# Kernel tuning notes

Hardware: AMD Instinct MI355X
Metric: run time of the kernel (lower is better)

Reference implementation:

```python
import jax, jax.numpy as jnp
import numpy as np

N_EMB = 1024
N_HEADS = 16
HS = N_EMB // N_HEADS  # 64
BASE = 10000.0


def _rope_cache(T):
    # theta uses dim = n_emb (as in the source), sliced to hs//2 frequencies
    i = jnp.arange(HS // 2, dtype=jnp.float32)
    theta = BASE ** (-2.0 * i / N_EMB)            # [hs/2]
    pos = jnp.arange(T, dtype=jnp.float32)        # [T]
    ang = pos[:, None] * theta[None, :]           # [T, hs/2]
    return jnp.cos(ang), jnp.sin(ang)


def _apply_rope(x, cos, sin):
    # x: [B, T, nh, hs]; rotate consecutive pairs along hs
    b, t, nh, hs = x.shape
    xr = x.reshape(b, t, nh, hs // 2, 2)
    c = cos[None, :, None, :]
    s = sin[None, :, None, :]
    r0 = xr[..., 0] * c - xr[..., 1] * s
    r1 = xr[..., 1] * c + xr[..., 0] * s
    return jnp.stack([r0, r1], axis=-1).reshape(b, t, nh, hs)


def setup_inputs() -> dict:
    key = jax.random.key(0)
    k1, k2, k3, k4 = jax.random.split(key, 4)
    B, T = 2, 2048
    w_std = 0.02
    x = jax.random.normal(k1, (B, T, N_EMB), jnp.float32)
    Wq = jax.random.normal(k2, (N_EMB, N_EMB), jnp.float32) * w_std
    Wk = jax.random.normal(k3, (N_EMB, N_EMB), jnp.float32) * w_std
    Wv = jax.random.normal(k4, (N_EMB, N_EMB), jnp.float32) * w_std
    return {"x": x, "Wq": Wq, "Wk": Wk, "Wv": Wv}


def reference(x, Wq, Wk, Wv):
    B, T, C = x.shape
    # nn.Linear(bias=False): y = x @ W.T
    q = (x @ Wq.T).reshape(B, T, N_HEADS, HS)
    k = (x @ Wk.T).reshape(B, T, N_HEADS, HS)
    v = (x @ Wv.T).reshape(B, T, N_HEADS, HS)
    cos, sin = _rope_cache(T)
    q = _apply_rope(q, cos, sin)
    k = _apply_rope(k, cos, sin)
    # scale uses C (n_emb), as in the source (not head_size)
    wei = jnp.einsum('bqhd,bkhd->bhqk', q, k) * (C ** -0.5)  # [B, nh, T, T]
    mask = jnp.tril(jnp.ones((T, T), dtype=bool))
    wei = jnp.where(mask[None, None], wei, -jnp.inf)
    wei = jax.nn.softmax(wei, axis=-1)
    # dropout is identity in eval mode
    out = jnp.einsum('bhqk,bkhd->bqhd', wei, v).reshape(B, T, C)
    return out
```

## Files before the change

kernel.cpp:

```cpp
#include <hip/hip_runtime.h>
#include <stdint.h>

typedef unsigned short u16;
typedef __bf16 bf16x8 __attribute__((ext_vector_type(8)));
typedef unsigned short u16x8 __attribute__((ext_vector_type(8)));
typedef unsigned short u16x4 __attribute__((ext_vector_type(4)));
typedef float f32x4 __attribute__((ext_vector_type(4)));
typedef uint32_t u32v4 __attribute__((ext_vector_type(4)));

#define LOG2E 1.4426950408889634f

typedef const __attribute__((address_space(1))) uint32_t as1_u32;
typedef __attribute__((address_space(3))) uint32_t as3_u32;

__device__ __forceinline__ u16 f2bf(float f) {
  union { float f; uint32_t i; } v; v.f = f;
  uint32_t r = (v.i + 0x7fffu + ((v.i >> 16) & 1u)) >> 16;
  return (u16)r;
}
__device__ __forceinline__ float bf2f(u16 u) {
  union { uint32_t i; float f; } v; v.i = ((uint32_t)u) << 16; return v.f;
}

__device__ __forceinline__ void gld_lds16(const void* g, void* l) {
  as1_u32* gp = (as1_u32*)((uintptr_t)g);
  as3_u32* lp = (as3_u32*)(uint32_t)(uintptr_t)(l);
  __builtin_amdgcn_global_load_lds(gp, lp, 16, 0, 0);
}

__global__ __launch_bounds__(256) void f32_to_bf16(
    const float* __restrict__ x, const float* __restrict__ wq,
    const float* __restrict__ wk, const float* __restrict__ wv,
    u16* __restrict__ xc, u16* __restrict__ wqc,
    u16* __restrict__ wkc, u16* __restrict__ wvc) {
  const int z = blockIdx.y;
  const float* src = z == 0 ? x : (z == 1 ? wq : (z == 2 ? wk : wv));
  u16* dst = z == 0 ? xc : (z == 1 ? wqc : (z == 2 ? wkc : wvc));
  const int n = z == 0 ? (1 << 22) : (1 << 20);

  const int idx = (blockIdx.x * 256 + (int)threadIdx.x) * 8;
  if (idx >= n) return;
  const f32x4 a = *(const f32x4*)&src[idx];
  const f32x4 b = *(const f32x4*)&src[idx + 4];
  u16x8 o;
#pragma unroll
  for (int j = 0; j < 4; j++) { o[j] = f2bf(a[j]); o[j + 4] = f2bf(b[j]); }
  *(u16x8*)&dst[idx] = o;
}

__global__ __launch_bounds__(256) void qkv_gemm(
    const u16* __restrict__ xc, const u16* __restrict__ wqc,
    const u16* __restrict__ wkc, const u16* __restrict__ wvc,
    u16* __restrict__ qo, u16* __restrict__ ko, u16* __restrict__ vt) {
  __shared__ __align__(16) u16 As[128 * 32];
  __shared__ __align__(16) u16 Bs[128 * 32];

  const int tid = threadIdx.x;
  const int lane = tid & 63;
  const int w = tid >> 6;
  const int wm = w >> 1, wn = w & 1;
  const int quad = lane >> 4, m16 = lane & 15;
  const int which = blockIdx.z;

  const u16* __restrict__ Ap;
  const u16* __restrict__ Bp;
  int m0, n0;
  if (which == 2) {
    Ap = wvc; Bp = xc;
    m0 = blockIdx.x * 128;
    n0 = blockIdx.y * 128;
  } else {
    Ap = xc; Bp = which == 0 ? wqc : wkc;
    m0 = blockIdx.y * 128;
    n0 = blockIdx.x * 128;
  }

  const f32x4 z4 = {0.f, 0.f, 0.f, 0.f};
  f32x4 acc[4][4];
#pragma unroll
  for (int i = 0; i < 4; i++)
#pragma unroll
    for (int j = 0; j < 4; j++) acc[i][j] = z4;

  const int rowA = m0 + w * 32 + (lane >> 2);
  const int rowB = n0 + w * 32 + (lane >> 2);
  const int cch = (lane & 3) * 8;

  for (int k0 = 0; k0 < 1024; k0 += 32) {
    __syncthreads();
#pragma unroll
    for (int i = 0; i < 2; i++) {
      gld_lds16(&Ap[(size_t)(rowA + i * 16) * 1024 + k0 + cch],
                &As[(w * 32 + i * 16) * 32]);
      gld_lds16(&Bp[(size_t)(rowB + i * 16) * 1024 + k0 + cch],
                &Bs[(w * 32 + i * 16) * 32]);
    }
    __syncthreads();

    bf16x8 af[4], bfr[4];
#pragma unroll
    for (int t = 0; t < 4; t++) {
      af[t]  = *(const bf16x8*)&As[(wm * 64 + t * 16 + m16) * 32 + quad * 8];
      bfr[t] = *(const bf16x8*)&Bs[(wn * 64 + t * 16 + m16) * 32 + quad * 8];
    }
#pragma unroll
    for (int mt = 0; mt < 4; mt++)
#pragma unroll
      for (int nt = 0; nt < 4; nt++)
        acc[mt][nt] = __builtin_amdgcn_mfma_f32_16x16x32_bf16(
            af[mt], bfr[nt], acc[mt][nt], 0, 0, 0);
  }

  if (which < 2) {
    u16* __restrict__ out = which == 0 ? qo : ko;
#pragma unroll
    for (int mt = 0; mt < 4; mt++) {
      const int row = m0 + wm * 64 + mt * 16 + quad * 4;
#pragma unroll
      for (int nt = 0; nt < 4; nt++) {
        const int n = n0 + wn * 64 + nt * 16 + m16;
        f32x4 a = acc[mt][nt];
#pragma unroll
        for (int r = 0; r < 4; r++)
          out[(size_t)(row + r) * 1024 + n] = f2bf(a[r]);
      }
    }
  } else {
#pragma unroll
    for (int mt = 0; mt < 4; mt++) {
      const int row = m0 + wm * 64 + mt * 16 + quad * 4;
#pragma unroll
      for (int nt = 0; nt < 4; nt++) {
        const int n = n0 + wn * 64 + nt * 16 + m16;
        f32x4 a = acc[mt][nt];
#pragma unroll
        for (int r = 0; r < 4; r++)
          vt[(size_t)(row + r) * 4096 + n] = f2bf(a[r]);
      }
    }
  }
}

__global__ __launch_bounds__(256) void rope_inplace(u16* __restrict__ qb,
                                                    u16* __restrict__ kb) {
  u16* buf = blockIdx.y == 0 ? qb : kb;
  const int p = blockIdx.x * 256 + (int)threadIdx.x;
  const int nidx = p * 2;
  const int row = nidx >> 10;
  const int col = nidx & 1023;
  const int i = (col & 63) >> 1;
  const int t = row & 2047;
  const float theta = exp2f(-(float)i * 0.02595256324130752f);
  const float ang = (float)t * theta;
  float s, c;
  sincosf(ang, &s, &c);
  const float a0 = bf2f(buf[(size_t)row * 1024 + col]);
  const float a1 = bf2f(buf[(size_t)row * 1024 + col + 1]);
  buf[(size_t)row * 1024 + col]     = f2bf(a0 * c - a1 * s);
  buf[(size_t)row * 1024 + col + 1] = f2bf(a1 * c + a0 * s);
}

__global__ __launch_bounds__(256, 4) void flash_attn(
    const u16* __restrict__ qg, const u16* __restrict__ kg,
    const u16* __restrict__ vt, float* __restrict__ out) {
  __shared__ __align__(16) u16 Ks[128 * 72];
  __shared__ __align__(16) u16 Vs[64 * 136];

  const int tid = threadIdx.x, lane = tid & 63, w = tid >> 6;
  const int quad = lane >> 4, m16 = lane & 15;

  const int id  = (int)blockIdx.x;
  const int wid = (id & 7) * 128 + (id >> 3);
  const int uu  = wid & 31;
  const int v   = wid >> 5;
  const int qt  = (v & 1) ? (31 - uu) : uu;
  const int h   = v & 15;
  const int b   = v >> 4;

  const size_t base = (size_t)b * 2048 * 1024 + (size_t)h * 64;
  const size_t vbase = (size_t)(h * 64) * 4096 + (size_t)b * 2048;
  const float SC = 0.03125f * LOG2E;

  const f32x4 z4 = {0.f, 0.f, 0.f, 0.f};
  const int srow = tid >> 2, sc = (tid & 3) * 16;

  union { u16x8 u; bf16x8 f; } ones;
#pragma unroll
  for (int j = 0; j < 8; j++) ones.u[j] = 0x3F80;

  const int q0 = qt * 64;
  const int nr = (qt + 2) >> 1;

  const u16* qsrc = &qg[base + (size_t)(q0 + w * 16 + m16) * 1024 + quad * 8];
  const bf16x8 qf0 = *(const bf16x8*)qsrc;
  const bf16x8 qf1 = *(const bf16x8*)(qsrc + 32);

  u16x8 kr0, kr1, kr2, kr3, vr0, vr1, vr2, vr3;
  {
    const u16* ks = &kg[base + (size_t)srow * 1024 + sc];
    kr0 = *(const u16x8*)ks; kr1 = *(const u16x8*)(ks + 8);
    const u16* ks2 = ks + (size_t)64 * 1024;
    kr2 = *(const u16x8*)ks2; kr3 = *(const u16x8*)(ks2 + 8);
    const u16* vs = &vt[vbase + (size_t)srow * 4096 + sc];
    vr0 = *(const u16x8*)vs; vr1 = *(const u16x8*)(vs + 8);
    vr2 = *(const u16x8*)(vs + 64); vr3 = *(const u16x8*)(vs + 72);
  }

  f32x4 l4 = z4;
  f32x4 O[4];
#pragma unroll
  for (int d = 0; d < 4; d++) O[d] = z4;

  const int qrow0 = q0 + w * 16 + quad * 4;
  const int qcol  = q0 + w * 16 + m16;

  for (int rr = 0; rr < nr; ++rr) {
    const int k0 = rr * 128;
    if (rr) __syncthreads();
    *(u16x8*)&Ks[srow * 72 + sc] = kr0;
    *(u16x8*)&Ks[srow * 72 + sc + 8] = kr1;
    *(u16x8*)&Ks[(64 + srow) * 72 + sc] = kr2;
    *(u16x8*)&Ks[(64 + srow) * 72 + sc + 8] = kr3;
    {
      const u16x4* v0 = (const u16x4*)&vr0;
      const u16x4* v1 = (const u16x4*)&vr1;
      *(u16x4*)&Vs[srow * 136 + sc]      = v0[0];
      *(u16x4*)&Vs[srow * 136 + sc + 4]  = v1[0];
      *(u16x4*)&Vs[srow * 136 + sc + 8]  = v0[1];
      *(u16x4*)&Vs[srow * 136 + sc + 12] = v1[1];
      const u16x4* v2 = (const u16x4*)&vr2;
      const u16x4* v3 = (const u16x4*)&vr3;
      *(u16x4*)&Vs[srow * 136 + 64 + sc]      = v2[0];
      *(u16x4*)&Vs[srow * 136 + 64 + sc + 4]  = v3[0];
      *(u16x4*)&Vs[srow * 136 + 64 + sc + 8]  = v2[1];
      *(u16x4*)&Vs[srow * 136 + 64 + sc + 12] = v3[1];
    }
    __syncthreads();
    if (rr + 1 < nr) {
      const u16* ks = &kg[base + (size_t)(k0 + 128 + srow) * 1024 + sc];
      kr0 = *(const u16x8*)ks; kr1 = *(const u16x8*)(ks + 8);
      const u16* ks2 = ks + (size_t)64 * 1024;
      kr2 = *(const u16x8*)ks2; kr3 = *(const u16x8*)(ks2 + 8);
      const u16* vs = &vt[vbase + (size_t)srow * 4096 + k0 + 128 + sc];
      vr0 = *(const u16x8*)vs; vr1 = *(const u16x8*)(vs + 8);
      vr2 = *(const u16x8*)(vs + 64); vr3 = *(const u16x8*)(vs + 72);
    }

    f32x4 S[8];
#pragma unroll
    for (int nt = 0; nt < 8; nt++) {
      const bf16x8 kf0 = *(const bf16x8*)&Ks[(nt * 16 + m16) * 72 + quad * 8];
      const bf16x8 kf1 =
          *(const bf16x8*)&Ks[(nt * 16 + m16) * 72 + 32 + quad * 8];
      S[nt] = __builtin_amdgcn_mfma_f32_16x16x32_bf16(kf0, qf0, z4, 0, 0, 0);
      S[nt] = __builtin_amdgcn_mfma_f32_16x16x32_bf16(kf1, qf1, S[nt], 0, 0, 0);
    }

    const bool lastr = (rr == nr - 1);
    uint32_t W[16];
#pragma unroll
    for (int nt = 0; nt < 8; nt++) {
      float p[4];
#pragma unroll
      for (int r = 0; r < 4; r++) {
        float e = exp2f(S[nt][r] * SC);
        const int key = k0 + nt * 16 + quad * 4 + r;
        if (lastr && key > qcol) e = 0.f;
        p[r] = e;
      }
      uint32_t w0, w1;
      asm("v_cvt_pk_bf16_f32 %0, %1, %2" : "=v"(w0) : "v"(p[0]), "v"(p[1]));
      asm("v_cvt_pk_bf16_f32 %0, %1, %2" : "=v"(w1) : "v"(p[2]), "v"(p[3]));
      W[2 * nt] = w0; W[2 * nt + 1] = w1;
    }

    union { u32v4 u; bf16x8 f; } P[4];
#pragma unroll
    for (int ks = 0; ks < 4; ks++) {
      uint32_t a0 = W[4 * ks], b0 = W[4 * ks + 2];
      uint32_t a1 = W[4 * ks + 1], b1 = W[4 * ks + 3];
      asm("v_permlane32_swap_b32 %0, %1" : "+v"(a0), "+v"(b0));
      asm("v_permlane32_swap_b32 %0, %1" : "+v"(a1), "+v"(b1));
      P[ks].u = (u32v4){a0, a1, b0, b1};
    }

#pragma unroll
    for (int ks = 0; ks < 4; ks++)
      l4 = __builtin_amdgcn_mfma_f32_16x16x32_bf16(P[ks].f, ones.f, l4,
                                                   0, 0, 0);

#pragma unroll
    for (int dt = 0; dt < 4; dt++) {
#pragma unroll
      for (int ks = 0; ks < 4; ks++) {
        const bf16x8 vf =
            *(const bf16x8*)&Vs[(dt * 16 + m16) * 136 + ks * 32 + quad * 8];
        O[dt] = __builtin_amdgcn_mfma_f32_16x16x32_bf16(P[ks].f, vf, O[dt],
                                                        0, 0, 0);
      }
    }
  }

  float inv[4];
#pragma unroll
  for (int r = 0; r < 4; r++) inv[r] = 1.0f / l4[r];

#pragma unroll
  for (int dt = 0; dt < 4; dt++)
#pragma unroll
    for (int r = 0; r < 4; r++)
      out[base + (size_t)(qrow0 + r) * 1024 + dt * 16 + m16] =
          O[dt][r] * inv[r];
}

extern "C" void kernel_launch(void* const* d_in, const int* in_sizes, int n_in,
                              void* d_out, int out_size, void* d_ws, size_t ws_size,
                              hipStream_t stream) {
  const float* x  = (const float*)d_in[0];
  const float* Wq = (const float*)d_in[1];
  const float* Wk = (const float*)d_in[2];
  const float* Wv = (const float*)d_in[3];
  u16* qb  = (u16*)d_ws;
  u16* kb  = qb  + (size_t)4096 * 1024;
  u16* vtw = kb  + (size_t)4096 * 1024;
  u16* xc  = vtw + (size_t)4096 * 1024;
  u16* wqc = xc  + (size_t)4096 * 1024;
  u16* wkc = wqc + (size_t)1024 * 1024;
  u16* wvc = wkc + (size_t)1024 * 1024;

  f32_to_bf16<<<dim3(2048, 4), 256, 0, stream>>>(x, Wq, Wk, Wv,
                                                 xc, wqc, wkc, wvc);
  qkv_gemm<<<dim3(8, 32, 3), 256, 0, stream>>>(xc, wqc, wkc, wvc,
                                               qb, kb, vtw);
  rope_inplace<<<dim3(8192, 2), 256, 0, stream>>>(qb, kb);
  flash_attn<<<dim3(1024, 1, 1), 256, 0, stream>>>(qb, kb, vtw, (float*)d_out);
}
```

Baseline: 165.8 us.

## Drop LDS staging in flash attention, use single-wave blocks reading K/V from global

The attention kernel moves from 256-thread blocks that stage K and V tiles through shared memory to 64-thread single-wave blocks that load MFMA fragments straight from global memory (relying on cache), and the grid grows fourfold. Each wave now computes its own causal trip count, which removes barriers and LDS traffic and trims per-wave work on the diagonal. The V-transpose store in the GEMM permutes key columns so that the direct global fragment loads line up with the P layout produced by the permlane swap. The risk is heavier L2/global traffic, because each wave re-reads K/V that the four waves of a block previously shared.

```diff
diff --git a/kernel.cpp b/kernel.cpp
--- a/kernel.cpp
+++ b/kernel.cpp
@@ -126,12 +126,13 @@
       }
     }
   } else {
+    const int m16p = (m16 & 3) | ((m16 & 4) << 1) | ((m16 & 8) >> 1);
 #pragma unroll
     for (int mt = 0; mt < 4; mt++) {
       const int row = m0 + wm * 64 + mt * 16 + quad * 4;
 #pragma unroll
       for (int nt = 0; nt < 4; nt++) {
-        const int n = n0 + wn * 64 + nt * 16 + m16;
+        const int n = n0 + wn * 64 + nt * 16 + m16p;
         f32x4 a = acc[mt][nt];
 #pragma unroll
         for (int r = 0; r < 4; r++)
@@ -160,98 +161,56 @@
   buf[(size_t)row * 1024 + col + 1] = f2bf(a1 * c + a0 * s);
 }
 
-__global__ __launch_bounds__(256, 4) void flash_attn(
+__global__ __launch_bounds__(64, 4) void flash_attn(
     const u16* __restrict__ qg, const u16* __restrict__ kg,
     const u16* __restrict__ vt, float* __restrict__ out) {
-  __shared__ __align__(16) u16 Ks[128 * 72];
-  __shared__ __align__(16) u16 Vs[64 * 136];
-
-  const int tid = threadIdx.x, lane = tid & 63, w = tid >> 6;
+  const int lane = threadIdx.x;
   const int quad = lane >> 4, m16 = lane & 15;
 
-  const int id  = (int)blockIdx.x;
-  const int wid = (id & 7) * 128 + (id >> 3);
-  const int uu  = wid & 31;
-  const int v   = wid >> 5;
-  const int qt  = (v & 1) ? (31 - uu) : uu;
-  const int h   = v & 15;
-  const int b   = v >> 4;
-
-  const size_t base = (size_t)b * 2048 * 1024 + (size_t)h * 64;
+  const int id   = (int)blockIdx.x;
+  const int X    = id & 7;
+  const int rem  = id >> 3;
+  const int c    = rem & 31;
+  const int j    = rem >> 5;
+  const int vloc = j & 3;
+  const int ws   = j >> 2;
+  const int qt   = (vloc & 1) ? (31 - c) : c;
+  const int v    = X * 4 + vloc;
+  const int h    = v & 15;
+  const int b    = v >> 4;
+
+  const size_t base  = (size_t)b * 2048 * 1024 + (size_t)h * 64;
   const size_t vbase = (size_t)(h * 64) * 4096 + (size_t)b * 2048;
   const float SC = 0.03125f * LOG2E;
-
   const f32x4 z4 = {0.f, 0.f, 0.f, 0.f};
-  const int srow = tid >> 2, sc = (tid & 3) * 16;
 
   union { u16x8 u; bf16x8 f; } ones;
 #pragma unroll
-  for (int j = 0; j < 8; j++) ones.u[j] = 0x3F80;
-
-  const int q0 = qt * 64;
-  const int nr = (qt + 2) >> 1;
-
-  const u16* qsrc = &qg[base + (size_t)(q0 + w * 16 + m16) * 1024 + quad * 8];
+  for (int k = 0; k < 8; k++) ones.u[k] = 0x3F80;
+
+  const int q0    = qt * 64;
+  const int qrow0 = q0 + ws * 16 + quad * 4;
+  const int qcol  = q0 + ws * 16 + m16;
+  const int nr    = ((q0 + ws * 16 + 15) >> 7) + 1;
+
+  const u16* qsrc = &qg[base + (size_t)(q0 + ws * 16 + m16) * 1024 + quad * 8];
   const bf16x8 qf0 = *(const bf16x8*)qsrc;
   const bf16x8 qf1 = *(const bf16x8*)(qsrc + 32);
 
-  u16x8 kr0, kr1, kr2, kr3, vr0, vr1, vr2, vr3;
-  {
-    const u16* ks = &kg[base + (size_t)srow * 1024 + sc];
-    kr0 = *(const u16x8*)ks; kr1 = *(const u16x8*)(ks + 8);
-    const u16* ks2 = ks + (size_t)64 * 1024;
-    kr2 = *(const u16x8*)ks2; kr3 = *(const u16x8*)(ks2 + 8);
-    const u16* vs = &vt[vbase + (size_t)srow * 4096 + sc];
-    vr0 = *(const u16x8*)vs; vr1 = *(const u16x8*)(vs + 8);
-    vr2 = *(const u16x8*)(vs + 64); vr3 = *(const u16x8*)(vs + 72);
-  }
-
   f32x4 l4 = z4;
   f32x4 O[4];
 #pragma unroll
   for (int d = 0; d < 4; d++) O[d] = z4;
 
-  const int qrow0 = q0 + w * 16 + quad * 4;
-  const int qcol  = q0 + w * 16 + m16;
-
   for (int rr = 0; rr < nr; ++rr) {
     const int k0 = rr * 128;
-    if (rr) __syncthreads();
-    *(u16x8*)&Ks[srow * 72 + sc] = kr0;
-    *(u16x8*)&Ks[srow * 72 + sc + 8] = kr1;
-    *(u16x8*)&Ks[(64 + srow) * 72 + sc] = kr2;
-    *(u16x8*)&Ks[(64 + srow) * 72 + sc + 8] = kr3;
-    {
-      const u16x4* v0 = (const u16x4*)&vr0;
-      const u16x4* v1 = (const u16x4*)&vr1;
-      *(u16x4*)&Vs[srow * 136 + sc]      = v0[0];
-      *(u16x4*)&Vs[srow * 136 + sc + 4]  = v1[0];
-      *(u16x4*)&Vs[srow * 136 + sc + 8]  = v0[1];
-      *(u16x4*)&Vs[srow * 136 + sc + 12] = v1[1];
-      const u16x4* v2 = (const u16x4*)&vr2;
-      const u16x4* v3 = (const u16x4*)&vr3;
-      *(u16x4*)&Vs[srow * 136 + 64 + sc]      = v2[0];
-      *(u16x4*)&Vs[srow * 136 + 64 + sc + 4]  = v3[0];
-      *(u16x4*)&Vs[srow * 136 + 64 + sc + 8]  = v2[1];
-      *(u16x4*)&Vs[srow * 136 + 64 + sc + 12] = v3[1];
-    }
-    __syncthreads();
-    if (rr + 1 < nr) {
-      const u16* ks = &kg[base + (size_t)(k0 + 128 + srow) * 1024 + sc];
-      kr0 = *(const u16x8*)ks; kr1 = *(const u16x8*)(ks + 8);
-      const u16* ks2 = ks + (size_t)64 * 1024;
-      kr2 = *(const u16x8*)ks2; kr3 = *(const u16x8*)(ks2 + 8);
-      const u16* vs = &vt[vbase + (size_t)srow * 4096 + k0 + 128 + sc];
-      vr0 = *(const u16x8*)vs; vr1 = *(const u16x8*)(vs + 8);
-      vr2 = *(const u16x8*)(vs + 64); vr3 = *(const u16x8*)(vs + 72);
-    }
 
     f32x4 S[8];
 #pragma unroll
     for (int nt = 0; nt < 8; nt++) {
-      const bf16x8 kf0 = *(const bf16x8*)&Ks[(nt * 16 + m16) * 72 + quad * 8];
-      const bf16x8 kf1 =
-          *(const bf16x8*)&Ks[(nt * 16 + m16) * 72 + 32 + quad * 8];
+      const u16* kp = &kg[base + (size_t)(k0 + nt * 16 + m16) * 1024 + quad * 8];
+      const bf16x8 kf0 = *(const bf16x8*)kp;
+      const bf16x8 kf1 = *(const bf16x8*)(kp + 32);
       S[nt] = __builtin_amdgcn_mfma_f32_16x16x32_bf16(kf0, qf0, z4, 0, 0, 0);
       S[nt] = __builtin_amdgcn_mfma_f32_16x16x32_bf16(kf1, qf1, S[nt], 0, 0, 0);
     }
@@ -293,8 +252,8 @@
     for (int dt = 0; dt < 4; dt++) {
 #pragma unroll
       for (int ks = 0; ks < 4; ks++) {
-        const bf16x8 vf =
-            *(const bf16x8*)&Vs[(dt * 16 + m16) * 136 + ks * 32 + quad * 8];
+        const bf16x8 vf = *(const bf16x8*)
+            &vt[vbase + (size_t)(dt * 16 + m16) * 4096 + k0 + ks * 32 + quad * 8];
         O[dt] = __builtin_amdgcn_mfma_f32_16x16x32_bf16(P[ks].f, vf, O[dt],
                                                         0, 0, 0);
       }
@@ -333,5 +292,5 @@
   qkv_gemm<<<dim3(8, 32, 3), 256, 0, stream>>>(xc, wqc, wkc, wvc,
                                                qb, kb, vtw);
   rope_inplace<<<dim3(8192, 2), 256, 0, stream>>>(qb, kb);
-  flash_attn<<<dim3(1024, 1, 1), 256, 0, stream>>>(qb, kb, vtw, (float*)d_out);
-}
+  flash_attn<<<dim3(4096, 1, 1), 64, 0, stream>>>(qb, kb, vtw, (float*)d_out);
+}
```

Result: slower. 262.7 us (+58.4%).
